# Kernel tuning notes

Hardware: AMD Instinct MI355X
Metric: run time of the kernel (lower is better)

Reference implementation:

```python
import jax, jax.numpy as jnp
import numpy as np

EMBED_DIM = 768
NUM_HEADS = 12
HEAD_DIM = EMBED_DIM // NUM_HEADS
BSZ = 8
N_NODE = 512


def setup_inputs() -> dict:
    key = jax.random.key(0)
    ks = jax.random.split(key, 12)
    s = 0.02
    E = EMBED_DIM
    return {
        "query": jax.random.normal(ks[0], (N_NODE, BSZ, E), jnp.float32),
        "attention_bias": jax.random.normal(ks[1], (BSZ, NUM_HEADS, N_NODE, N_NODE), jnp.float32),
        "node_position": jax.random.normal(ks[2], (BSZ, N_NODE, 3), jnp.float32),
        "Wq": jax.random.normal(ks[3], (E, E), jnp.float32) * s,
        "bq": jnp.zeros((E,), jnp.float32),
        "Wk": jax.random.normal(ks[4], (E, E), jnp.float32) * s,
        "bk": jnp.zeros((E,), jnp.float32),
        "Wv": jax.random.normal(ks[5], (E, E), jnp.float32) * s,
        "bv": jnp.zeros((E,), jnp.float32),
        "W1": jax.random.normal(ks[6], (E, 1), jnp.float32) * s,
        "b1": jnp.zeros((1,), jnp.float32),
        "W2": jax.random.normal(ks[7], (E, 1), jnp.float32) * s,
        "b2": jnp.zeros((1,), jnp.float32),
        "W3": jax.random.normal(ks[8], (E, 1), jnp.float32) * s,
        "b3": jnp.zeros((1,), jnp.float32),
    }


def reference(query, attention_bias, node_position, Wq, bq, Wk, bk, Wv, bv,
              W1, b1, W2, b2, W3, b3):
    bsz, n = node_position.shape[:2]
    H = attention_bias.shape[1]
    E = query.shape[-1]
    hd = E // H
    scaling = hd ** -0.5

    # unit direction vectors between node pairs: delta[b,i,j] = pos[j]-pos[i]
    delta = node_position[:, None, :, :] - node_position[:, :, None, :]  # (b,n,n,3)
    dist = jnp.linalg.norm(delta, axis=-1)                               # (b,n,n)
    delta = delta / (dist[..., None] + 1e-5)

    x = jnp.swapaxes(query, 0, 1)  # (b,n,E)
    q = (x @ Wq + bq).reshape(bsz, n, H, hd).transpose(0, 2, 1, 3) * scaling  # (b,h,n,d)
    k = (x @ Wk + bk).reshape(bsz, n, H, hd).transpose(0, 2, 1, 3)
    v = (x @ Wv + bv).reshape(bsz, n, H, hd).transpose(0, 2, 1, 3)

    attn = jnp.einsum('bhid,bhjd->bhij', q, k)
    probs = jax.nn.softmax(attn + attention_bias, axis=-1)  # (b,h,i,j); dropout = identity (eval)

    # rotational aggregation: out[b,i,c,h,d] = sum_j probs[b,h,i,j]*delta[b,i,j,c]*v[b,h,j,d]
    xo = jnp.einsum('bhij,bijc,bhjd->bichd', probs, delta, v).reshape(bsz, n, 3, E)

    f1 = xo[:, :, 0, :] @ W1 + b1  # (b,n,1)
    f2 = xo[:, :, 1, :] @ W2 + b2
    f3 = xo[:, :, 2, :] @ W3 + b3
    return jnp.concatenate([f1, f2, f3], axis=-1).astype(jnp.float32)  # (b,n,3)
```

## Files before the change

kernel.cpp:

```cpp
#include <hip/hip_runtime.h>
#include <math.h>

#define EDIM 768
#define NH 12
#define HD 64
#define BSZ 8
#define NN 512
#define NCAT 1664

typedef short short8 __attribute__((ext_vector_type(8)));
typedef float f32x4 __attribute__((ext_vector_type(4)));

__device__ __forceinline__ unsigned short f2bf(float x) {
    unsigned int u = __float_as_uint(x);
    u = (u + 0x7FFF + ((u >> 16) & 1)) >> 16;
    return (unsigned short)u;
}
__device__ __forceinline__ float bf2f(unsigned short s) {
    return __uint_as_float(((unsigned int)s) << 16);
}
__device__ __forceinline__ void gl2lds16(const void* g, void* l) {
    __builtin_amdgcn_global_load_lds(
        (const __attribute__((address_space(1))) unsigned int*)g,
        (__attribute__((address_space(3))) unsigned int*)l, 16, 0, 0);
}

__global__ void k_init_out(float* __restrict__ out, const float* b1, const float* b2, const float* b3) {
    int idx = blockIdx.x * 256 + threadIdx.x;
    if (idx < BSZ * NN * 3) {
        int c = idx % 3;
        out[idx] = (c == 0) ? b1[0] : (c == 1) ? b2[0] : b3[0];
    }
}

__global__ void k_build_wcat(float* __restrict__ Wcat,
                             const float* __restrict__ Wq, const float* __restrict__ Wk,
                             const float* __restrict__ Wv,
                             const float* __restrict__ W1, const float* __restrict__ W2,
                             const float* __restrict__ W3) {
    int idx = blockIdx.x * 256 + threadIdx.x;
    if (idx >= EDIM * NCAT) return;
    int e = idx / NCAT, o = idx - (idx / NCAT) * NCAT;
    float v = 0.f;
    if (o < 768) {
        v = Wq[e * EDIM + o];
    } else if (o < 1536) {
        v = Wk[e * EDIM + (o - 768)];
    } else if (o < 1572) {
        int o2 = o - 1536;
        int h = o2 / 3, c = o2 - (o2 / 3) * 3;
        const float* Wc = (c == 0) ? W1 : (c == 1) ? W2 : W3;
        float s = 0.f;
        #pragma unroll 8
        for (int d = 0; d < HD; d++) s += Wv[e * EDIM + h * HD + d] * Wc[h * HD + d];
        v = s;
    }
    Wcat[idx] = v;
}

__global__ void k_build_bcat(float* __restrict__ bcat,
                             const float* __restrict__ bq, const float* __restrict__ bk,
                             const float* __restrict__ bv,
                             const float* __restrict__ W1, const float* __restrict__ W2,
                             const float* __restrict__ W3) {
    int o = blockIdx.x * 256 + threadIdx.x;
    if (o >= NCAT) return;
    float v = 0.f;
    if (o < 768) v = bq[o];
    else if (o < 1536) v = bk[o - 768];
    else if (o < 1572) {
        int o2 = o - 1536;
        int h = o2 / 3, c = o2 - (o2 / 3) * 3;
        const float* Wc = (c == 0) ? W1 : (c == 1) ? W2 : W3;
        float s = 0.f;
        for (int d = 0; d < HD; d++) s += bv[h * HD + d] * Wc[h * HD + d];
        v = s;
    }
    bcat[o] = v;
}

__global__ __launch_bounds__(256) void k_transpose_wcat(const float* __restrict__ Wcat,
                                                        unsigned short* __restrict__ WT) {
    __shared__ float tile[32][33];
    const int tx = threadIdx.x & 31, ty = threadIdx.x >> 5;
    const int n0 = blockIdx.x * 32, e0 = blockIdx.y * 32;
    #pragma unroll
    for (int s = 0; s < 4; s++)
        tile[ty + s * 8][tx] = Wcat[(size_t)(e0 + ty + s * 8) * NCAT + n0 + tx];
    __syncthreads();
    #pragma unroll
    for (int s = 0; s < 4; s++)
        WT[(size_t)(n0 + ty + s * 8) * EDIM + e0 + tx] = f2bf(tile[tx][ty + s * 8]);
}

__global__ __launch_bounds__(256) void k_cvt_x(const float* __restrict__ q, unsigned short* __restrict__ Xb) {
    int idx = blockIdx.x * 256 + threadIdx.x;
    int m = idx / 96, e8 = (idx - (idx / 96) * 96) * 8;
    int b = m >> 9, i = m & (NN - 1);
    const float* src = q + ((size_t)i * BSZ + b) * EDIM + e8;
    float4 v0 = *(const float4*)src;
    float4 v1 = *(const float4*)(src + 4);
    unsigned int p0 = f2bf(v0.x) | ((unsigned int)f2bf(v0.y) << 16);
    unsigned int p1 = f2bf(v0.z) | ((unsigned int)f2bf(v0.w) << 16);
    unsigned int p2 = f2bf(v1.x) | ((unsigned int)f2bf(v1.y) << 16);
    unsigned int p3 = f2bf(v1.z) | ((unsigned int)f2bf(v1.w) << 16);
    uint4 pk = {p0, p1, p2, p3};
    *(uint4*)&Xb[(size_t)idx * 8] = pk;
}

__global__ __launch_bounds__(256) void k_geom(const float* __restrict__ pos,
                                              unsigned short* __restrict__ ud0,
                                              unsigned short* __restrict__ ud1,
                                              unsigned short* __restrict__ ud2) {
    __shared__ float psx[NN], psy[NN], psz[NN];
    const int bid = blockIdx.x;
    const int b = bid >> 6, i0 = (bid & 63) * 8;
    const int t = threadIdx.x;
    for (int idx = t; idx < NN; idx += 256) {
        const float* p = pos + ((size_t)b * NN + idx) * 3;
        psx[idx] = p[0]; psy[idx] = p[1]; psz[idx] = p[2];
    }
    __syncthreads();
    const int i = i0 + (t >> 5);
    const float qx = psx[i], qy = psy[i], qz = psz[i];
    const size_t row = ((size_t)b * NN + i) * NN;
    for (int jt = 0; jt < 4; jt++) {
        int j = ((t & 31) + jt * 32) * 4;
        unsigned int o0[2], o1[2], o2[2];
        unsigned short s0[4], s1[4], s2[4];
        #pragma unroll
        for (int u = 0; u < 4; u++) {
            float dx = psx[j + u] - qx, dy = psy[j + u] - qy, dz = psz[j + u] - qz;
            float inv = 1.f / (sqrtf(dx * dx + dy * dy + dz * dz) + 1e-5f);
            s0[u] = f2bf(dx * inv); s1[u] = f2bf(dy * inv); s2[u] = f2bf(dz * inv);
        }
        o0[0] = s0[0] | ((unsigned)s0[1] << 16); o0[1] = s0[2] | ((unsigned)s0[3] << 16);
        o1[0] = s1[0] | ((unsigned)s1[1] << 16); o1[1] = s1[2] | ((unsigned)s1[3] << 16);
        o2[0] = s2[0] | ((unsigned)s2[1] << 16); o2[1] = s2[2] | ((unsigned)s2[3] << 16);
        *(uint2*)&ud0[row + j] = make_uint2(o0[0], o0[1]);
        *(uint2*)&ud1[row + j] = make_uint2(o1[0], o1[1]);
        *(uint2*)&ud2[row + j] = make_uint2(o2[0], o2[1]);
    }
}

__global__ __launch_bounds__(256) void k_gemm_qkv(
        const unsigned short* __restrict__ Xb, const unsigned short* __restrict__ WT,
        const float* __restrict__ bcat,
        unsigned short* __restrict__ qb, unsigned short* __restrict__ kb,
        float* __restrict__ vwb) {
    __shared__ short As[8 * 128 * 8];
    __shared__ short Bs[8 * 128 * 8];
    const int t = threadIdx.x;
    const int m0 = blockIdx.x * 128, n0 = blockIdx.y * 128;
    const int w = t >> 6, lane = t & 63, quad = lane >> 4, ln = lane & 15;
    const int wm = (w & 1) * 64, wn = (w >> 1) * 64;

    f32x4 acc[4][4];
    #pragma unroll
    for (int mi = 0; mi < 4; mi++)
        #pragma unroll
        for (int ni = 0; ni < 4; ni++) acc[mi][ni] = (f32x4){0.f, 0.f, 0.f, 0.f};

    for (int k0 = 0; k0 < EDIM; k0 += 64) {
        __syncthreads();
        #pragma unroll
        for (int is = 0; is < 4; is++) {
            int slot = is * 256 + t;
            int g = slot >> 7, m = slot & 127;
            gl2lds16(Xb + (size_t)(m0 + m) * EDIM + k0 + g * 8, &As[(size_t)(is * 256 + w * 64) * 8]);
        }
        #pragma unroll
        for (int is = 0; is < 4; is++) {
            int slot = is * 256 + t;
            int g = slot >> 7, n = slot & 127;
            gl2lds16(WT + (size_t)(n0 + n) * EDIM + k0 + g * 8, &Bs[(size_t)(is * 256 + w * 64) * 8]);
        }
        __syncthreads();
        #pragma unroll
        for (int s = 0; s < 2; s++) {
            short8 af[4], bf[4];
            #pragma unroll
            for (int mi = 0; mi < 4; mi++)
                af[mi] = *(const short8*)&As[(size_t)((s * 4 + quad) * 128 + wm + mi * 16 + ln) * 8];
            #pragma unroll
            for (int ni = 0; ni < 4; ni++)
                bf[ni] = *(const short8*)&Bs[(size_t)((s * 4 + quad) * 128 + wn + ni * 16 + ln) * 8];
            #pragma unroll
            for (int mi = 0; mi < 4; mi++)
                #pragma unroll
                for (int ni = 0; ni < 4; ni++)
                    acc[mi][ni] = __builtin_amdgcn_mfma_f32_16x16x32_bf16(af[mi], bf[ni], acc[mi][ni], 0, 0, 0);
        }
    }

    #pragma unroll
    for (int mi = 0; mi < 4; mi++) {
        #pragma unroll
        for (int r = 0; r < 4; r++) {
            int mg = m0 + wm + mi * 16 + quad * 4 + r;
            int b_ = mg >> 9, i_ = mg & (NN - 1);
            #pragma unroll
            for (int ni = 0; ni < 4; ni++) {
                int o = n0 + wn + ni * 16 + ln;
                float val = acc[mi][ni][r] + bcat[o];
                if (o < 768) {
                    int h = o >> 6, d = o & 63;
                    qb[(((size_t)b_ * NH + h) * NN + i_) * HD + d] = f2bf(val * 0.125f);
                } else if (o < 1536) {
                    int o2 = o - 768;
                    int h = o2 >> 6, d = o2 & 63;
                    kb[(((size_t)b_ * NH + h) * NN + i_) * HD + d] = f2bf(val);
                } else if (o < 1572) {
                    int o2 = o - 1536;
                    int h = o2 / 3, c = o2 - (o2 / 3) * 3;
                    vwb[(((size_t)b_ * NH + h) * NN + i_) * 3 + c] = val;
                }
            }
        }
    }
}

__global__ __launch_bounds__(256) void k_attn(
        const unsigned short* __restrict__ qb, const unsigned short* __restrict__ kb,
        const float* __restrict__ vwb, const float* __restrict__ bias,
        const unsigned short* __restrict__ ud0, const unsigned short* __restrict__ ud1,
        const unsigned short* __restrict__ ud2, float* __restrict__ out) {
    __shared__ short Ks[8 * 64 * 8];
    __shared__ float ws0[NN], ws1[NN], ws2[NN];

    const int t = threadIdx.x;
    const int bid = blockIdx.x;
    const int h = bid % NH;
    const int it = (bid / NH) & 7;
    const int b = bid / (NH * 8);
    const int i0 = it * 64;
    const int w = t >> 6, lane = t & 63, quad = lane >> 4, ln = lane & 15;
    const size_t bh = (size_t)b * NH + h;

    for (int idx = t; idx < NN * 3; idx += 256) {
        float v = vwb[bh * (NN * 3) + idx];
        int j = idx / 3, c = idx - (idx / 3) * 3;
        if (c == 0) ws0[j] = v; else if (c == 1) ws1[j] = v; else ws2[j] = v;
    }

    const int ig = i0 + w * 16 + ln;
    const unsigned short* qrow = qb + (bh * NN + ig) * HD;
    short8 qf0 = *(const short8*)(qrow + quad * 8);
    short8 qf1 = *(const short8*)(qrow + 32 + quad * 8);
    const float* brow = bias + (bh * NN + ig) * NN;
    const size_t udrow = ((size_t)b * NN + ig) * NN;

    float m_r = -3.0e38f, l_r = 0.f, a0 = 0.f, a1 = 0.f, a2 = 0.f;

    for (int jt = 0; jt < 8; jt++) {
        const int j0 = jt * 64;
        __syncthreads();
        #pragma unroll
        for (int is = 0; is < 2; is++) {
            int slot = is * 256 + t;
            int dg = slot >> 6, j = slot & 63;
            gl2lds16(kb + (bh * NN + j0 + j) * HD + dg * 8, &Ks[(size_t)(is * 256 + w * 64) * 8]);
        }
        __syncthreads();

        f32x4 acc[4];
        #pragma unroll
        for (int sub = 0; sub < 4; sub++) {
            short8 af0 = *(const short8*)&Ks[(size_t)(quad * 64 + sub * 16 + ln) * 8];
            short8 af1 = *(const short8*)&Ks[(size_t)((4 + quad) * 64 + sub * 16 + ln) * 8];
            f32x4 z = {0.f, 0.f, 0.f, 0.f};
            z = __builtin_amdgcn_mfma_f32_16x16x32_bf16(af0, qf0, z, 0, 0, 0);
            z = __builtin_amdgcn_mfma_f32_16x16x32_bf16(af1, qf1, z, 0, 0, 0);
            acc[sub] = z;
        }

        float sv[16];
        #pragma unroll
        for (int sub = 0; sub < 4; sub++) {
            f32x4 bv = *(const f32x4*)(brow + j0 + sub * 16 + quad * 4);
            sv[sub * 4 + 0] = acc[sub][0] + bv[0];
            sv[sub * 4 + 1] = acc[sub][1] + bv[1];
            sv[sub * 4 + 2] = acc[sub][2] + bv[2];
            sv[sub * 4 + 3] = acc[sub][3] + bv[3];
        }
        float lm = sv[0];
        #pragma unroll
        for (int u = 1; u < 16; u++) lm = fmaxf(lm, sv[u]);
        float mn = fmaxf(m_r, lm);
        float alpha = __expf(m_r - mn);
        float lp = 0.f, s0 = 0.f, s1 = 0.f, s2 = 0.f;
        #pragma unroll
        for (int sub = 0; sub < 4; sub++) {
            int j = j0 + sub * 16 + quad * 4;
            f32x4 w0v = *(const f32x4*)&ws0[j];
            f32x4 w1v = *(const f32x4*)&ws1[j];
            f32x4 w2v = *(const f32x4*)&ws2[j];
            union { uint2 u; unsigned short s[4]; } U0, U1, U2;
            U0.u = *(const uint2*)&ud0[udrow + j];
            U1.u = *(const uint2*)&ud1[udrow + j];
            U2.u = *(const uint2*)&ud2[udrow + j];
            #pragma unroll
            for (int r = 0; r < 4; r++) {
                float p = __expf(sv[sub * 4 + r] - mn);
                lp += p;
                s0 = fmaf(p * bf2f(U0.s[r]), w0v[r], s0);
                s1 = fmaf(p * bf2f(U1.s[r]), w1v[r], s1);
                s2 = fmaf(p * bf2f(U2.s[r]), w2v[r], s2);
            }
        }
        l_r = l_r * alpha + lp;
        a0 = a0 * alpha + s0;
        a1 = a1 * alpha + s1;
        a2 = a2 * alpha + s2;
        m_r = mn;
    }

    #pragma unroll
    for (int off = 16; off <= 32; off <<= 1) {
        float mo = __shfl_xor(m_r, off, 64);
        float lo = __shfl_xor(l_r, off, 64);
        float b0 = __shfl_xor(a0, off, 64);
        float b1 = __shfl_xor(a1, off, 64);
        float b2 = __shfl_xor(a2, off, 64);
        float mn = fmaxf(m_r, mo);
        float e1 = __expf(m_r - mn), e2 = __expf(mo - mn);
        l_r = l_r * e1 + lo * e2;
        a0 = a0 * e1 + b0 * e2;
        a1 = a1 * e1 + b1 * e2;
        a2 = a2 * e1 + b2 * e2;
        m_r = mn;
    }
    if (quad == 0) {
        float inv = 1.f / l_r;
        float* op = out + ((size_t)b * NN + ig) * 3;
        atomicAdd(op + 0, a0 * inv);
        atomicAdd(op + 1, a1 * inv);
        atomicAdd(op + 2, a2 * inv);
    }
}

extern "C" void kernel_launch(void* const* d_in, const int* in_sizes, int n_in,
                              void* d_out, int out_size, void* d_ws, size_t ws_size,
                              hipStream_t stream) {
    const float* query = (const float*)d_in[0];
    const float* bias  = (const float*)d_in[1];
    const float* pos   = (const float*)d_in[2];
    const float* Wq = (const float*)d_in[3];
    const float* bq = (const float*)d_in[4];
    const float* Wk = (const float*)d_in[5];
    const float* bk = (const float*)d_in[6];
    const float* Wv = (const float*)d_in[7];
    const float* bv = (const float*)d_in[8];
    const float* W1 = (const float*)d_in[9];
    const float* b1 = (const float*)d_in[10];
    const float* W2 = (const float*)d_in[11];
    const float* b2 = (const float*)d_in[12];
    const float* W3 = (const float*)d_in[13];
    const float* b3 = (const float*)d_in[14];
    float* out = (float*)d_out;

    char* p = (char*)d_ws;
    float* Wcat = (float*)p;                 p += (size_t)EDIM * NCAT * 4;
    float* bcat = (float*)p;                 p += (size_t)NCAT * 4 + 256;
    unsigned short* WT = (unsigned short*)p; p += (size_t)NCAT * EDIM * 2;
    unsigned short* Xb = (unsigned short*)p; p += (size_t)BSZ * NN * EDIM * 2;
    unsigned short* qb = (unsigned short*)p; p += (size_t)BSZ * NH * NN * HD * 2;
    unsigned short* kb = (unsigned short*)p; p += (size_t)BSZ * NH * NN * HD * 2;
    float* vwb = (float*)p;                  p += (size_t)BSZ * NH * NN * 3 * 4;
    unsigned short* ud0 = (unsigned short*)p; p += (size_t)BSZ * NN * NN * 2;
    unsigned short* ud1 = (unsigned short*)p; p += (size_t)BSZ * NN * NN * 2;
    unsigned short* ud2 = (unsigned short*)p; p += (size_t)BSZ * NN * NN * 2;

    k_init_out<<<(BSZ * NN * 3 + 255) / 256, 256, 0, stream>>>(out, b1, b2, b3);
    k_build_wcat<<<(EDIM * NCAT + 255) / 256, 256, 0, stream>>>(Wcat, Wq, Wk, Wv, W1, W2, W3);
    k_build_bcat<<<(NCAT + 255) / 256, 256, 0, stream>>>(bcat, bq, bk, bv, W1, W2, W3);
    dim3 gt(NCAT / 32, EDIM / 32);
    k_transpose_wcat<<<gt, 256, 0, stream>>>(Wcat, WT);
    k_cvt_x<<<(BSZ * NN * 96) / 256, 256, 0, stream>>>(query, Xb);
    k_geom<<<BSZ * 64, 256, 0, stream>>>(pos, ud0, ud1, ud2);
    dim3 g2(32, 13);
    k_gemm_qkv<<<g2, 256, 0, stream>>>(Xb, WT, bcat, qb, kb, vwb);
    k_attn<<<BSZ * 8 * NH, 256, 0, stream>>>(qb, kb, vwb, bias, ud0, ud1, ud2, out);
}
```

Before: 269.5 us.

## Fuse prep kernels, split attention over key chunks, halve GEMM M tile

Merges the weight build, transpose, x conversion, geometry and bias setup into one multi-role prep kernel. It writes bf16 WT directly, with no fp32 Wcat staging and no separate init kernel. The attention kernel now splits the key dimension into four chunks, giving four times as many blocks. Each block writes partial max, sum and accumulators, and a new finalize kernel merges them and replaces the atomics. The QKV GEMM M tile drops from 128 to 64 to double its grid. Together these cut launch count and extra memory passes and raise occupancy, at the cost of partial-result traffic and an extra kernel.

```diff
diff --git a/kernel.cpp b/kernel.cpp
--- a/kernel.cpp
+++ b/kernel.cpp
@@ -25,121 +25,110 @@
         (__attribute__((address_space(3))) unsigned int*)l, 16, 0, 0);
 }
 
-__global__ void k_init_out(float* __restrict__ out, const float* b1, const float* b2, const float* b3) {
-    int idx = blockIdx.x * 256 + threadIdx.x;
-    if (idx < BSZ * NN * 3) {
-        int c = idx % 3;
-        out[idx] = (c == 0) ? b1[0] : (c == 1) ? b2[0] : b3[0];
-    }
-}
-
-__global__ void k_build_wcat(float* __restrict__ Wcat,
-                             const float* __restrict__ Wq, const float* __restrict__ Wk,
-                             const float* __restrict__ Wv,
-                             const float* __restrict__ W1, const float* __restrict__ W2,
-                             const float* __restrict__ W3) {
-    int idx = blockIdx.x * 256 + threadIdx.x;
-    if (idx >= EDIM * NCAT) return;
-    int e = idx / NCAT, o = idx - (idx / NCAT) * NCAT;
-    float v = 0.f;
-    if (o < 768) {
-        v = Wq[e * EDIM + o];
-    } else if (o < 1536) {
-        v = Wk[e * EDIM + (o - 768)];
-    } else if (o < 1572) {
-        int o2 = o - 1536;
+#define PB_GEOM_END 512
+#define PB_TR_END   1664
+#define PB_VW_END   1772
+#define PB_CVT_END  3308
+#define PB_BC_END   3315
+#define PREP_BLOCKS 3350
+
+__global__ __launch_bounds__(256) void k_prep(
+        const float* __restrict__ query, const float* __restrict__ pos,
+        const float* __restrict__ Wq, const float* __restrict__ bq,
+        const float* __restrict__ Wk, const float* __restrict__ bk,
+        const float* __restrict__ Wv, const float* __restrict__ bv,
+        const float* __restrict__ W1, const float* __restrict__ W2,
+        const float* __restrict__ W3,
+        unsigned short* __restrict__ WT, float* __restrict__ bcat,
+        unsigned short* __restrict__ Xb,
+        unsigned short* __restrict__ ud0, unsigned short* __restrict__ ud1,
+        unsigned short* __restrict__ ud2) {
+    __shared__ float sm[1536];
+    const int bid = blockIdx.x;
+    const int t = threadIdx.x;
+
+    if (bid < PB_GEOM_END) {
+        float* psx = sm; float* psy = sm + NN; float* psz = sm + 2 * NN;
+        const int b = bid >> 6, i0 = (bid & 63) * 8;
+        for (int idx = t; idx < NN; idx += 256) {
+            const float* p = pos + ((size_t)b * NN + idx) * 3;
+            psx[idx] = p[0]; psy[idx] = p[1]; psz[idx] = p[2];
+        }
+        __syncthreads();
+        const int i = i0 + (t >> 5);
+        const float qx = psx[i], qy = psy[i], qz = psz[i];
+        const size_t row = ((size_t)b * NN + i) * NN;
+        for (int jt = 0; jt < 4; jt++) {
+            int j = ((t & 31) + jt * 32) * 4;
+            unsigned short s0[4], s1[4], s2[4];
+            #pragma unroll
+            for (int u = 0; u < 4; u++) {
+                float dx = psx[j + u] - qx, dy = psy[j + u] - qy, dz = psz[j + u] - qz;
+                float inv = 1.f / (sqrtf(dx * dx + dy * dy + dz * dz) + 1e-5f);
+                s0[u] = f2bf(dx * inv); s1[u] = f2bf(dy * inv); s2[u] = f2bf(dz * inv);
+            }
+            *(uint2*)&ud0[row + j] = make_uint2(s0[0] | ((unsigned)s0[1] << 16), s0[2] | ((unsigned)s0[3] << 16));
+            *(uint2*)&ud1[row + j] = make_uint2(s1[0] | ((unsigned)s1[1] << 16), s1[2] | ((unsigned)s1[3] << 16));
+            *(uint2*)&ud2[row + j] = make_uint2(s2[0] | ((unsigned)s2[1] << 16), s2[2] | ((unsigned)s2[3] << 16));
+        }
+    } else if (bid < PB_TR_END) {
+        float (*tile)[33] = (float(*)[33])sm;
+        const int tb = bid - PB_GEOM_END;
+        const int n0 = (tb % 48) * 32, e0 = (tb / 48) * 32;
+        const float* src = (n0 < 768) ? Wq : Wk;
+        const int ol0 = (n0 < 768) ? n0 : (n0 - 768);
+        const int tx = t & 31, ty = t >> 5;
+        #pragma unroll
+        for (int s = 0; s < 4; s++)
+            tile[ty + s * 8][tx] = src[(size_t)(e0 + ty + s * 8) * EDIM + ol0 + tx];
+        __syncthreads();
+        #pragma unroll
+        for (int s = 0; s < 4; s++)
+            WT[(size_t)(n0 + ty + s * 8) * EDIM + e0 + tx] = f2bf(tile[tx][ty + s * 8]);
+    } else if (bid < PB_VW_END) {
+        int idx = (bid - PB_TR_END) * 256 + t;
+        int o2 = idx / 768, e = idx - o2 * 768;
         int h = o2 / 3, c = o2 - (o2 / 3) * 3;
         const float* Wc = (c == 0) ? W1 : (c == 1) ? W2 : W3;
         float s = 0.f;
         #pragma unroll 8
-        for (int d = 0; d < HD; d++) s += Wv[e * EDIM + h * HD + d] * Wc[h * HD + d];
-        v = s;
-    }
-    Wcat[idx] = v;
-}
-
-__global__ void k_build_bcat(float* __restrict__ bcat,
-                             const float* __restrict__ bq, const float* __restrict__ bk,
-                             const float* __restrict__ bv,
-                             const float* __restrict__ W1, const float* __restrict__ W2,
-                             const float* __restrict__ W3) {
-    int o = blockIdx.x * 256 + threadIdx.x;
-    if (o >= NCAT) return;
-    float v = 0.f;
-    if (o < 768) v = bq[o];
-    else if (o < 1536) v = bk[o - 768];
-    else if (o < 1572) {
-        int o2 = o - 1536;
-        int h = o2 / 3, c = o2 - (o2 / 3) * 3;
-        const float* Wc = (c == 0) ? W1 : (c == 1) ? W2 : W3;
-        float s = 0.f;
-        for (int d = 0; d < HD; d++) s += bv[h * HD + d] * Wc[h * HD + d];
-        v = s;
-    }
-    bcat[o] = v;
-}
-
-__global__ __launch_bounds__(256) void k_transpose_wcat(const float* __restrict__ Wcat,
-                                                        unsigned short* __restrict__ WT) {
-    __shared__ float tile[32][33];
-    const int tx = threadIdx.x & 31, ty = threadIdx.x >> 5;
-    const int n0 = blockIdx.x * 32, e0 = blockIdx.y * 32;
-    #pragma unroll
-    for (int s = 0; s < 4; s++)
-        tile[ty + s * 8][tx] = Wcat[(size_t)(e0 + ty + s * 8) * NCAT + n0 + tx];
-    __syncthreads();
-    #pragma unroll
-    for (int s = 0; s < 4; s++)
-        WT[(size_t)(n0 + ty + s * 8) * EDIM + e0 + tx] = f2bf(tile[tx][ty + s * 8]);
-}
-
-__global__ __launch_bounds__(256) void k_cvt_x(const float* __restrict__ q, unsigned short* __restrict__ Xb) {
-    int idx = blockIdx.x * 256 + threadIdx.x;
-    int m = idx / 96, e8 = (idx - (idx / 96) * 96) * 8;
-    int b = m >> 9, i = m & (NN - 1);
-    const float* src = q + ((size_t)i * BSZ + b) * EDIM + e8;
-    float4 v0 = *(const float4*)src;
-    float4 v1 = *(const float4*)(src + 4);
-    unsigned int p0 = f2bf(v0.x) | ((unsigned int)f2bf(v0.y) << 16);
-    unsigned int p1 = f2bf(v0.z) | ((unsigned int)f2bf(v0.w) << 16);
-    unsigned int p2 = f2bf(v1.x) | ((unsigned int)f2bf(v1.y) << 16);
-    unsigned int p3 = f2bf(v1.z) | ((unsigned int)f2bf(v1.w) << 16);
-    uint4 pk = {p0, p1, p2, p3};
-    *(uint4*)&Xb[(size_t)idx * 8] = pk;
-}
-
-__global__ __launch_bounds__(256) void k_geom(const float* __restrict__ pos,
-                                              unsigned short* __restrict__ ud0,
-                                              unsigned short* __restrict__ ud1,
-                                              unsigned short* __restrict__ ud2) {
-    __shared__ float psx[NN], psy[NN], psz[NN];
-    const int bid = blockIdx.x;
-    const int b = bid >> 6, i0 = (bid & 63) * 8;
-    const int t = threadIdx.x;
-    for (int idx = t; idx < NN; idx += 256) {
-        const float* p = pos + ((size_t)b * NN + idx) * 3;
-        psx[idx] = p[0]; psy[idx] = p[1]; psz[idx] = p[2];
-    }
-    __syncthreads();
-    const int i = i0 + (t >> 5);
-    const float qx = psx[i], qy = psy[i], qz = psz[i];
-    const size_t row = ((size_t)b * NN + i) * NN;
-    for (int jt = 0; jt < 4; jt++) {
-        int j = ((t & 31) + jt * 32) * 4;
-        unsigned int o0[2], o1[2], o2[2];
-        unsigned short s0[4], s1[4], s2[4];
-        #pragma unroll
-        for (int u = 0; u < 4; u++) {
-            float dx = psx[j + u] - qx, dy = psy[j + u] - qy, dz = psz[j + u] - qz;
-            float inv = 1.f / (sqrtf(dx * dx + dy * dy + dz * dz) + 1e-5f);
-            s0[u] = f2bf(dx * inv); s1[u] = f2bf(dy * inv); s2[u] = f2bf(dz * inv);
-        }
-        o0[0] = s0[0] | ((unsigned)s0[1] << 16); o0[1] = s0[2] | ((unsigned)s0[3] << 16);
-        o1[0] = s1[0] | ((unsigned)s1[1] << 16); o1[1] = s1[2] | ((unsigned)s1[3] << 16);
-        o2[0] = s2[0] | ((unsigned)s2[1] << 16); o2[1] = s2[2] | ((unsigned)s2[3] << 16);
-        *(uint2*)&ud0[row + j] = make_uint2(o0[0], o0[1]);
-        *(uint2*)&ud1[row + j] = make_uint2(o1[0], o1[1]);
-        *(uint2*)&ud2[row + j] = make_uint2(o2[0], o2[1]);
+        for (int d = 0; d < HD; d++) s += Wv[(size_t)e * EDIM + h * HD + d] * Wc[h * HD + d];
+        WT[(size_t)(1536 + o2) * EDIM + e] = f2bf(s);
+    } else if (bid < PB_CVT_END) {
+        int idx = (bid - PB_VW_END) * 256 + t;
+        int m = idx / 96, e8 = (idx - (idx / 96) * 96) * 8;
+        int b = m >> 9, i = m & (NN - 1);
+        const float* src = query + ((size_t)i * BSZ + b) * EDIM + e8;
+        float4 v0 = *(const float4*)src;
+        float4 v1 = *(const float4*)(src + 4);
+        unsigned int p0 = f2bf(v0.x) | ((unsigned int)f2bf(v0.y) << 16);
+        unsigned int p1 = f2bf(v0.z) | ((unsigned int)f2bf(v0.w) << 16);
+        unsigned int p2 = f2bf(v1.x) | ((unsigned int)f2bf(v1.y) << 16);
+        unsigned int p3 = f2bf(v1.z) | ((unsigned int)f2bf(v1.w) << 16);
+        uint4 pk = {p0, p1, p2, p3};
+        *(uint4*)&Xb[(size_t)idx * 8] = pk;
+    } else if (bid < PB_BC_END) {
+        int o = (bid - PB_CVT_END) * 256 + t;
+        if (o < NCAT) {
+            float v = 0.f;
+            if (o < 768) v = bq[o];
+            else if (o < 1536) v = bk[o - 768];
+            else if (o < 1572) {
+                int o2 = o - 1536;
+                int h = o2 / 3, c = o2 - (o2 / 3) * 3;
+                const float* Wc = (c == 0) ? W1 : (c == 1) ? W2 : W3;
+                float s = 0.f;
+                for (int d = 0; d < HD; d++) s += bv[h * HD + d] * Wc[h * HD + d];
+                v = s;
+            }
+            bcat[o] = v;
+        }
+    } else {
+        int tid = (bid - PB_BC_END) * 256 + t;
+        if (tid < 8832) {
+            uint4 z = {0, 0, 0, 0};
+            *(uint4*)&WT[(size_t)1572 * EDIM + (size_t)tid * 8] = z;
+        }
     }
 }
 
@@ -148,25 +137,25 @@
         const float* __restrict__ bcat,
         unsigned short* __restrict__ qb, unsigned short* __restrict__ kb,
         float* __restrict__ vwb) {
-    __shared__ short As[8 * 128 * 8];
+    __shared__ short As[8 * 64 * 8];
     __shared__ short Bs[8 * 128 * 8];
     const int t = threadIdx.x;
-    const int m0 = blockIdx.x * 128, n0 = blockIdx.y * 128;
+    const int m0 = blockIdx.x * 64, n0 = blockIdx.y * 128;
     const int w = t >> 6, lane = t & 63, quad = lane >> 4, ln = lane & 15;
-    const int wm = (w & 1) * 64, wn = (w >> 1) * 64;
-
-    f32x4 acc[4][4];
+    const int wm = (w & 1) * 32, wn = (w >> 1) * 64;
+
+    f32x4 acc[2][4];
     #pragma unroll
-    for (int mi = 0; mi < 4; mi++)
+    for (int mi = 0; mi < 2; mi++)
         #pragma unroll
         for (int ni = 0; ni < 4; ni++) acc[mi][ni] = (f32x4){0.f, 0.f, 0.f, 0.f};
 
     for (int k0 = 0; k0 < EDIM; k0 += 64) {
         __syncthreads();
         #pragma unroll
-        for (int is = 0; is < 4; is++) {
+        for (int is = 0; is < 2; is++) {
             int slot = is * 256 + t;
-            int g = slot >> 7, m = slot & 127;
+            int g = slot >> 6, m = slot & 63;
             gl2lds16(Xb + (size_t)(m0 + m) * EDIM + k0 + g * 8, &As[(size_t)(is * 256 + w * 64) * 8]);
         }
         #pragma unroll
@@ -178,15 +167,15 @@
         __syncthreads();
         #pragma unroll
         for (int s = 0; s < 2; s++) {
-            short8 af[4], bf[4];
-            #pragma unroll
-            for (int mi = 0; mi < 4; mi++)
-                af[mi] = *(const short8*)&As[(size_t)((s * 4 + quad) * 128 + wm + mi * 16 + ln) * 8];
+            short8 af[2], bf[4];
+            #pragma unroll
+            for (int mi = 0; mi < 2; mi++)
+                af[mi] = *(const short8*)&As[(size_t)((s * 4 + quad) * 64 + wm + mi * 16 + ln) * 8];
             #pragma unroll
             for (int ni = 0; ni < 4; ni++)
                 bf[ni] = *(const short8*)&Bs[(size_t)((s * 4 + quad) * 128 + wn + ni * 16 + ln) * 8];
             #pragma unroll
-            for (int mi = 0; mi < 4; mi++)
+            for (int mi = 0; mi < 2; mi++)
                 #pragma unroll
                 for (int ni = 0; ni < 4; ni++)
                     acc[mi][ni] = __builtin_amdgcn_mfma_f32_16x16x32_bf16(af[mi], bf[ni], acc[mi][ni], 0, 0, 0);
@@ -194,7 +183,7 @@
     }
 
     #pragma unroll
-    for (int mi = 0; mi < 4; mi++) {
+    for (int mi = 0; mi < 2; mi++) {
         #pragma unroll
         for (int r = 0; r < 4; r++) {
             int mg = m0 + wm + mi * 16 + quad * 4 + r;
@@ -224,16 +213,21 @@
         const unsigned short* __restrict__ qb, const unsigned short* __restrict__ kb,
         const float* __restrict__ vwb, const float* __restrict__ bias,
         const unsigned short* __restrict__ ud0, const unsigned short* __restrict__ ud1,
-        const unsigned short* __restrict__ ud2, float* __restrict__ out) {
+        const unsigned short* __restrict__ ud2,
+        float* __restrict__ mp, float* __restrict__ lp,
+        float* __restrict__ a0p, float* __restrict__ a1p, float* __restrict__ a2p) {
     __shared__ short Ks[8 * 64 * 8];
     __shared__ float ws0[NN], ws1[NN], ws2[NN];
 
     const int t = threadIdx.x;
     const int bid = blockIdx.x;
     const int h = bid % NH;
-    const int it = (bid / NH) & 7;
-    const int b = bid / (NH * 8);
+    const int r1 = bid / NH;
+    const int js = r1 & 3;
+    const int it = (r1 >> 2) & 7;
+    const int b = r1 >> 5;
     const int i0 = it * 64;
+    const int jb = js * 128;
     const int w = t >> 6, lane = t & 63, quad = lane >> 4, ln = lane & 15;
     const size_t bh = (size_t)b * NH + h;
 
@@ -252,8 +246,8 @@
 
     float m_r = -3.0e38f, l_r = 0.f, a0 = 0.f, a1 = 0.f, a2 = 0.f;
 
-    for (int jt = 0; jt < 8; jt++) {
-        const int j0 = jt * 64;
+    for (int jt = 0; jt < 2; jt++) {
+        const int j0 = jb + jt * 64;
         __syncthreads();
         #pragma unroll
         for (int is = 0; is < 2; is++) {
@@ -288,7 +282,7 @@
         for (int u = 1; u < 16; u++) lm = fmaxf(lm, sv[u]);
         float mn = fmaxf(m_r, lm);
         float alpha = __expf(m_r - mn);
-        float lp = 0.f, s0 = 0.f, s1 = 0.f, s2 = 0.f;
+        float lps = 0.f, s0 = 0.f, s1 = 0.f, s2 = 0.f;
         #pragma unroll
         for (int sub = 0; sub < 4; sub++) {
             int j = j0 + sub * 16 + quad * 4;
@@ -302,13 +296,13 @@
             #pragma unroll
             for (int r = 0; r < 4; r++) {
                 float p = __expf(sv[sub * 4 + r] - mn);
-                lp += p;
+                lps += p;
                 s0 = fmaf(p * bf2f(U0.s[r]), w0v[r], s0);
                 s1 = fmaf(p * bf2f(U1.s[r]), w1v[r], s1);
                 s2 = fmaf(p * bf2f(U2.s[r]), w2v[r], s2);
             }
         }
-        l_r = l_r * alpha + lp;
+        l_r = l_r * alpha + lps;
         a0 = a0 * alpha + s0;
         a1 = a1 * alpha + s1;
         a2 = a2 * alpha + s2;
@@ -331,12 +325,48 @@
         m_r = mn;
     }
     if (quad == 0) {
-        float inv = 1.f / l_r;
-        float* op = out + ((size_t)b * NN + ig) * 3;
-        atomicAdd(op + 0, a0 * inv);
-        atomicAdd(op + 1, a1 * inv);
-        atomicAdd(op + 2, a2 * inv);
-    }
+        size_t o4 = (bh * NN + ig) * 4 + js;
+        mp[o4] = m_r; lp[o4] = l_r;
+        a0p[o4] = a0; a1p[o4] = a1; a2p[o4] = a2;
+    }
+}
+
+__global__ __launch_bounds__(256) void k_finalize(
+        const float* __restrict__ mp, const float* __restrict__ lp,
+        const float* __restrict__ a0p, const float* __restrict__ a1p,
+        const float* __restrict__ a2p,
+        const float* __restrict__ b1, const float* __restrict__ b2,
+        const float* __restrict__ b3, float* __restrict__ out) {
+    int idx = blockIdx.x * 256 + threadIdx.x;
+    int b = idx >> 9, i = idx & (NN - 1);
+    float s0 = 0.f, s1 = 0.f, s2 = 0.f;
+    #pragma unroll
+    for (int h = 0; h < NH; h++) {
+        size_t base = (((size_t)b * NH + h) * NN + i) * 4;
+        f32x4 mv = *(const f32x4*)&mp[base];
+        f32x4 lv = *(const f32x4*)&lp[base];
+        f32x4 A0 = *(const f32x4*)&a0p[base];
+        f32x4 A1 = *(const f32x4*)&a1p[base];
+        f32x4 A2 = *(const f32x4*)&a2p[base];
+        float M = fmaxf(fmaxf(mv[0], mv[1]), fmaxf(mv[2], mv[3]));
+        float L = 0.f, c0 = 0.f, c1 = 0.f, c2 = 0.f;
+        #pragma unroll
+        for (int js = 0; js < 4; js++) {
+            float e = __expf(mv[js] - M);
+            L = fmaf(e, lv[js], L);
+            c0 = fmaf(e, A0[js], c0);
+            c1 = fmaf(e, A1[js], c1);
+            c2 = fmaf(e, A2[js], c2);
+        }
+        float inv = 1.f / L;
+        s0 = fmaf(c0, inv, s0);
+        s1 = fmaf(c1, inv, s1);
+        s2 = fmaf(c2, inv, s2);
+    }
+    float* op = out + (size_t)idx * 3;
+    op[0] = s0 + b1[0];
+    op[1] = s1 + b2[0];
+    op[2] = s2 + b3[0];
 }
 
 extern "C" void kernel_launch(void* const* d_in, const int* in_sizes, int n_in,
@@ -360,9 +390,8 @@
     float* out = (float*)d_out;
 
     char* p = (char*)d_ws;
-    float* Wcat = (float*)p;                 p += (size_t)EDIM * NCAT * 4;
-    float* bcat = (float*)p;                 p += (size_t)NCAT * 4 + 256;
     unsigned short* WT = (unsigned short*)p; p += (size_t)NCAT * EDIM * 2;
+    float* bcat = (float*)p;                 p += (size_t)NCAT * 4;
     unsigned short* Xb = (unsigned short*)p; p += (size_t)BSZ * NN * EDIM * 2;
     unsigned short* qb = (unsigned short*)p; p += (size_t)BSZ * NH * NN * HD * 2;
     unsigned short* kb = (unsigned short*)p; p += (size_t)BSZ * NH * NN * HD * 2;
@@ -370,15 +399,18 @@
     unsigned short* ud0 = (unsigned short*)p; p += (size_t)BSZ * NN * NN * 2;
     unsigned short* ud1 = (unsigned short*)p; p += (size_t)BSZ * NN * NN * 2;
     unsigned short* ud2 = (unsigned short*)p; p += (size_t)BSZ * NN * NN * 2;
-
-    k_init_out<<<(BSZ * NN * 3 + 255) / 256, 256, 0, stream>>>(out, b1, b2, b3);
-    k_build_wcat<<<(EDIM * NCAT + 255) / 256, 256, 0, stream>>>(Wcat, Wq, Wk, Wv, W1, W2, W3);
-    k_build_bcat<<<(NCAT + 255) / 256, 256, 0, stream>>>(bcat, bq, bk, bv, W1, W2, W3);
-    dim3 gt(NCAT / 32, EDIM / 32);
-    k_transpose_wcat<<<gt, 256, 0, stream>>>(Wcat, WT);
-    k_cvt_x<<<(BSZ * NN * 96) / 256, 256, 0, stream>>>(query, Xb);
-    k_geom<<<BSZ * 64, 256, 0, stream>>>(pos, ud0, ud1, ud2);
-    dim3 g2(32, 13);
+    const size_t PSZ = (size_t)BSZ * NH * NN * 4;
+    float* mp  = (float*)p; p += PSZ * 4;
+    float* lp  = (float*)p; p += PSZ * 4;
+    float* a0p = (float*)p; p += PSZ * 4;
+    float* a1p = (float*)p; p += PSZ * 4;
+    float* a2p = (float*)p; p += PSZ * 4;
+
+    k_prep<<<PREP_BLOCKS, 256, 0, stream>>>(query, pos, Wq, bq, Wk, bk, Wv, bv,
+                                            W1, W2, W3, WT, bcat, Xb, ud0, ud1, ud2);
+    dim3 g2(64, 13);
     k_gemm_qkv<<<g2, 256, 0, stream>>>(Xb, WT, bcat, qb, kb, vwb);
-    k_attn<<<BSZ * 8 * NH, 256, 0, stream>>>(qb, kb, vwb, bias, ud0, ud1, ud2, out);
-}
+    k_attn<<<BSZ * NH * 8 * 4, 256, 0, stream>>>(qb, kb, vwb, bias, ud0, ud1, ud2,
+                                                 mp, lp, a0p, a1p, a2p);
+    k_finalize<<<BSZ * NN / 256, 256, 0, stream>>>(mp, lp, a0p, a1p, a2p, b1, b2, b3, out);
+}
```

Result: slower. 288.3 us (+6.9%).
